# Kernel optimization log

Measured on AMD Instinct MI355X. Metric: run time of the kernel, lower is better.

Reference implementation:

```python
import jax, jax.numpy as jnp
import numpy as np

EPS = 1e-5


def gcn_conv(x, W, b, src, dst):
    """PyG GCNConv: transform, add self-loops, symmetric norm, scatter-add, bias."""
    N = x.shape[0]
    h = x @ W  # [N, out]
    loop = jnp.arange(N)
    s = jnp.concatenate([src, loop])  # sources incl. self-loops
    d = jnp.concatenate([dst, loop])  # targets incl. self-loops
    deg = jax.ops.segment_sum(jnp.ones(s.shape[0], h.dtype), d, num_segments=N)
    dis = jnp.where(deg > 0, jax.lax.rsqrt(deg), 0.0)  # deg^-1/2
    norm = dis[s] * dis[d]  # [E+N]
    out = jax.ops.segment_sum(h[s] * norm[:, None], d, num_segments=N)
    return out + b


def batchnorm(x, gamma, beta):
    mu = x.mean(axis=0)
    var = x.var(axis=0)
    return (x - mu) * jax.lax.rsqrt(var + EPS) * gamma + beta


def setup_inputs() -> dict:
    key = jax.random.key(0)
    ks = jax.random.split(key, 6)
    N, E = 100000, 1600000
    IN, HID, OUT = 128, 256, 64
    x = jax.random.normal(ks[0], (N, IN), dtype=jnp.float32)
    edge_index = jax.random.randint(ks[1], (2, E), 0, N, dtype=jnp.int64)
    W1 = jax.random.normal(ks[2], (IN, HID), dtype=jnp.float32) / np.sqrt(IN)
    b1 = jnp.zeros((HID,), jnp.float32)
    gamma1 = jnp.ones((HID,), jnp.float32)
    beta1 = jnp.zeros((HID,), jnp.float32)
    W2 = jax.random.normal(ks[3], (HID, OUT), dtype=jnp.float32) / np.sqrt(HID)
    b2 = jnp.zeros((OUT,), jnp.float32)
    return {"x": x, "edge_index": edge_index, "W1": W1, "b1": b1,
            "gamma1": gamma1, "beta1": beta1, "W2": W2, "b2": b2}


def reference(x, edge_index, W1, b1, gamma1, beta1, W2, b2):
    src, dst = edge_index[0], edge_index[1]
    h = gcn_conv(x, W1, b1, src, dst)
    h = jax.nn.relu(batchnorm(h, gamma1, beta1))
    # dropout is identity at inference
    return gcn_conv(h, W2, b2, src, dst)
```

## Files before the change

kernel.cpp:

```cpp
#include <hip/hip_runtime.h>
#include <hip/hip_bf16.h>


#define IN_F  128
#define HID_F 256
#define OUT_F 64
#define BK_SHIFT 8
#define BK_SIZE  256
#define CHUNK    8192
#define CAP      8192

typedef unsigned int uint;
typedef unsigned short ushort;
typedef short bf16x8 __attribute__((ext_vector_type(8)));
typedef float f32x4 __attribute__((ext_vector_type(4)));

__device__ __forceinline__ ushort f2bf(float f) {
    uint u = __float_as_uint(f);
    uint r = (u + 0x7fffu + ((u >> 16) & 1u)) >> 16;
    return (ushort)r;
}
__device__ __forceinline__ float bf_lo(uint u) { return __uint_as_float(u << 16); }
__device__ __forceinline__ float bf_hi(uint u) { return __uint_as_float(u & 0xffff0000u); }

#define ACC8(u)                                         \
    do {                                                \
        acc[0] += bf_lo((u).x); acc[1] += bf_hi((u).x); \
        acc[2] += bf_lo((u).y); acc[3] += bf_hi((u).y); \
        acc[4] += bf_lo((u).z); acc[5] += bf_hi((u).z); \
        acc[6] += bf_lo((u).w); acc[7] += bf_hi((u).w); \
    } while (0)


__global__ __launch_bounds__(512) void scatter_wprep_kernel(
        const int* __restrict__ src, const int* __restrict__ dst,
        int* __restrict__ bcursor, uint* __restrict__ ebuf,
        const float* __restrict__ W1, const float* __restrict__ W2,
        ushort* __restrict__ W1bp, ushort* __restrict__ W2bp,
        int E, int NB, int nchunk) {
    if (blockIdx.x >= nchunk) {
        int i = (blockIdx.x - nchunk) * 512 + threadIdx.x;
        if (i < 32768) {
            int kk = i & 31, c = (i >> 5) & 255, kc = i >> 13;
            W1bp[i] = f2bf(W1[(size_t)(kc * 32 + kk) * HID_F + c]);
        } else {
            int j = i - 32768;
            int kk = j & 31, c = (j >> 5) & 63, kc = j >> 11;
            W2bp[j] = f2bf(W2[(size_t)(kc * 32 + kk) * OUT_F + c]);
        }
        return;
    }
    __shared__ int h[512];
    __shared__ int cur[512];
    for (int i = threadIdx.x; i < NB; i += 512) h[i] = 0;
    __syncthreads();
    int base = blockIdx.x * CHUNK;
    int end = min(base + CHUNK, E);
    for (int i = base + threadIdx.x; i < end; i += 512)
        atomicAdd(&h[dst[i] >> BK_SHIFT], 1);
    __syncthreads();
    for (int i = threadIdx.x; i < NB; i += 512)
        cur[i] = i * CAP + (h[i] ? atomicAdd(&bcursor[i], h[i]) : 0);
    __syncthreads();
    for (int i = base + threadIdx.x; i < end; i += 512) {
        int d = dst[i], s = src[i];
        int b = d >> BK_SHIFT;
        int pos = atomicAdd(&cur[b], 1);
        ebuf[pos] = (uint)s | ((uint)(d & (BK_SIZE - 1)) << 24);
    }
}

__global__ __launch_bounds__(1024) void bucket_build_kernel(
        const uint* __restrict__ ebuf, const int* __restrict__ bcursor,
        int* __restrict__ deg_e, int* __restrict__ offsets,
        float* __restrict__ dis, int* __restrict__ ssrc, int N) {
    __shared__ int cnt[256], off[256], cur[256];
    int b = blockIdx.x;
    int t = threadIdx.x;
    if (t < 256) cnt[t] = 0;
    __syncthreads();
    int e0 = b * CAP;
    int e1 = e0 + min(bcursor[b], CAP);
    for (int i = e0 + t; i < e1; i += 1024)
        atomicAdd(&cnt[ebuf[i] >> 24], 1);
    __syncthreads();
    int v = (t < 256) ? cnt[t] : 0;
    int vpad = (v + 3) & ~3;
    if (t < 256) off[t] = vpad;
    __syncthreads();
    for (int o = 1; o < 256; o <<= 1) {
        int u = (t >= o && t < 256) ? off[t - o] : 0;
        __syncthreads();
        if (t < 256) off[t] += u;
        __syncthreads();
    }
    int base_pad = b * (CAP + 768);
    if (t < 256) {
        int excl = off[t] - vpad;
        int d = b * BK_SIZE + t;
        if (d < N) {
            deg_e[d] = vpad;
            offsets[d] = base_pad + excl;
            dis[d] = rsqrtf((float)(v + 1));
        }
        cur[t] = excl;
    }
    __syncthreads();
    for (int i = e0 + t; i < e1; i += 1024) {
        uint e = ebuf[i];
        int ld = e >> 24;
        int pos = atomicAdd(&cur[ld], 1);
        ssrc[base_pad + pos] = (int)(e & 0xFFFFFFu);
    }
    __syncthreads();
    if (t < 256) {
        int excl = off[t] - vpad;
        for (int i = v; i < vpad; i++)
            ssrc[base_pad + excl + i] = N;
    }
}

__global__ void xprep_kernel(const float* __restrict__ x, const float* __restrict__ dis,
                             uint* __restrict__ xs, int N) {
    int i = blockIdx.x * 256 + threadIdx.x;
    if (i < (N + 1) * 32) {
        int n = i >> 5;
        if (n >= N) { ((uint2*)xs)[i] = make_uint2(0u, 0u); return; }
        float dn = dis[n];
        float4 v = ((const float4*)x)[i];
        uint2 o;
        o.x = (uint)f2bf(dn * v.x) | ((uint)f2bf(dn * v.y) << 16);
        o.y = (uint)f2bf(dn * v.z) | ((uint)f2bf(dn * v.w) << 16);
        ((uint2*)xs)[i] = o;
    }
}


__global__ void aggx_kernel(const uint* __restrict__ xs, const int* __restrict__ ssrc,
                            const int* __restrict__ offsets, const int* __restrict__ deg_e,
                            const float* __restrict__ dis, uint* __restrict__ zb, int N) {
    int lane = threadIdx.x & 63;
    int n = blockIdx.x * 4 + (threadIdx.x >> 6);
    if (n >= N) return;
    int grp = lane >> 4;
    int ck = lane & 15;
    float acc[8];
#pragma unroll
    for (int i = 0; i < 8; i++) acc[i] = 0.f;
    int start = offsets[n], cnt = deg_e[n];
    for (int base = 0; base < cnt; base += 64) {
        int m = min(64, cnt - base);
        int idx = base + lane;
        int sv = ssrc[start + (idx < cnt ? idx : cnt - 1)];
        int rounds = m >> 2;
        int q = 0;
        for (; q + 4 <= rounds; q += 4) {
            int sA = __shfl(sv, ((q + 0) << 2) | grp);
            int sB = __shfl(sv, ((q + 1) << 2) | grp);
            int sC = __shfl(sv, ((q + 2) << 2) | grp);
            int sD = __shfl(sv, ((q + 3) << 2) | grp);
            uint4 uA = *(const uint4*)(xs + ((size_t)sA << 6) + (ck << 2));
            uint4 uB = *(const uint4*)(xs + ((size_t)sB << 6) + (ck << 2));
            uint4 uC = *(const uint4*)(xs + ((size_t)sC << 6) + (ck << 2));
            uint4 uD = *(const uint4*)(xs + ((size_t)sD << 6) + (ck << 2));
            ACC8(uA); ACC8(uB); ACC8(uC); ACC8(uD);
        }
        for (; q < rounds; q++) {
            int s = __shfl(sv, (q << 2) | grp);
            uint4 u = *(const uint4*)(xs + ((size_t)s << 6) + (ck << 2));
            ACC8(u);
        }
    }
#pragma unroll
    for (int i = 0; i < 8; i++) acc[i] += __shfl_down(acc[i], 32);
#pragma unroll
    for (int i = 0; i < 8; i++) acc[i] += __shfl_down(acc[i], 16);
    if (grp == 0) {
        uint4 u = *(const uint4*)(xs + ((size_t)n << 6) + (ck << 2));
        ACC8(u);
        float dn = dis[n];
        uint4 o;
        o.x = (uint)f2bf(dn * acc[0]) | ((uint)f2bf(dn * acc[1]) << 16);
        o.y = (uint)f2bf(dn * acc[2]) | ((uint)f2bf(dn * acc[3]) << 16);
        o.z = (uint)f2bf(dn * acc[4]) | ((uint)f2bf(dn * acc[5]) << 16);
        o.w = (uint)f2bf(dn * acc[6]) | ((uint)f2bf(dn * acc[7]) << 16);
        *(uint4*)(zb + ((size_t)n << 6) + (ck << 2)) = o;
    }
}

__global__ __launch_bounds__(256) void gemm1_kernel(const uint* __restrict__ zb,
                                                    const uint* __restrict__ W1bp,
                                                    const float* __restrict__ b1,
                                                    ushort* __restrict__ out1b,
                                                    float* __restrict__ bnp, int N) {
    __shared__ uint sbuf[8192];
    int t = threadIdx.x;
    int n0 = blockIdx.x * 64;
    for (int i = t; i < 64 * 16; i += 256) {
        int r = i >> 4, q = i & 15;
        int node = n0 + r;
        uint4 v = make_uint4(0u, 0u, 0u, 0u);
        if (node < N) v = *(const uint4*)(zb + (size_t)node * 64 + q * 4);
        int p = q ^ (r & 15);
        *(uint4*)(&sbuf[r * 64 + p * 4]) = v;
    }
    __syncthreads();
    int wave = t >> 6, lane = t & 63;
    int quad = lane >> 4, lrow = lane & 15;
    f32x4 acc[4][4];
#pragma unroll
    for (int m = 0; m < 4; m++)
#pragma unroll
        for (int nt = 0; nt < 4; nt++) acc[m][nt] = (f32x4)(0.f);
#pragma unroll
    for (int kc = 0; kc < 4; kc++) {
        bf16x8 bfr[4];
#pragma unroll
        for (int nt = 0; nt < 4; nt++) {
            int c = wave * 64 + nt * 16 + lrow;
            bfr[nt] = *(const bf16x8*)(W1bp + ((size_t)(kc * 256 + c) * 16 + quad * 4));
        }
        bf16x8 afr[4];
#pragma unroll
        for (int m = 0; m < 4; m++) {
            int p = (kc * 4 + quad) ^ lrow;
            afr[m] = *(const bf16x8*)(&sbuf[(m * 16 + lrow) * 64 + p * 4]);
        }
#pragma unroll
        for (int m = 0; m < 4; m++)
#pragma unroll
            for (int nt = 0; nt < 4; nt++)
                acc[m][nt] = __builtin_amdgcn_mfma_f32_16x16x32_bf16(
                    afr[m], bfr[nt], acc[m][nt], 0, 0, 0);
    }
    __syncthreads();
#pragma unroll
    for (int nt = 0; nt < 4; nt++) {
        int c = wave * 64 + nt * 16 + lrow;
        float bb = b1[c];
        float s = 0.f, q = 0.f;
#pragma unroll
        for (int m = 0; m < 4; m++) {
#pragma unroll
            for (int r = 0; r < 4; r++) {
                int row = m * 16 + quad * 4 + r;
                float v = acc[m][nt][r] + bb;
                if (n0 + row < N) { s += v; q = fmaf(v, v, q); }
                uint hv = (uint)f2bf(v);
                uint pv = __shfl_xor(hv, 1);
                if ((lrow & 1) == 0)
                    sbuf[row * 128 + (c >> 1)] = hv | (pv << 16);
            }
        }
        s += __shfl_down(s, 32); q += __shfl_down(q, 32);
        s += __shfl_down(s, 16); q += __shfl_down(q, 16);
        if (quad == 0) {
            bnp[(size_t)blockIdx.x * 512 + c] = s;
            bnp[(size_t)blockIdx.x * 512 + 256 + c] = q;
        }
    }
    __syncthreads();
    uint* out1g = (uint*)out1b;
    for (int i = t; i < 2048; i += 256) {
        int row = i >> 5;
        if (n0 + row < N)
            *(uint4*)(out1g + (size_t)(n0 + row) * 128 + (i & 31) * 4) =
                *(const uint4*)(&sbuf[i * 4]);
    }
}

__global__ void bnred_kernel(const float* __restrict__ bnp, float* __restrict__ bnsum,
                             int nblk) {
    int g = blockIdx.x, t = threadIdx.x;
    float s = 0.f, q = 0.f;
    for (int b = g; b < nblk; b += 32) {
        s += bnp[(size_t)b * 512 + t];
        q += bnp[(size_t)b * 512 + 256 + t];
    }
    atomicAdd(&bnsum[t], s);
    atomicAdd(&bnsum[256 + t], q);
}

__global__ __launch_bounds__(256) void gemm2_kernel(const ushort* __restrict__ out1b,
                                                    const uint* __restrict__ W2bp,
                                                    const float* __restrict__ dis,
                                                    const float* __restrict__ bnsum,
                                                    const float* __restrict__ gamma,
                                                    const float* __restrict__ beta,
                                                    ushort* __restrict__ gs, int N) {
    __shared__ uint sbuf[8192];
    __shared__ float bns[256], bnb[256];
    const uint* out1u = (const uint*)out1b;
    int t = threadIdx.x;
    int n0 = blockIdx.x * 64;
    if (blockIdx.x == 0 && t < 32) ((uint*)gs)[(size_t)N * 32 + t] = 0u;
    {
        float invN = 1.0f / (float)N;
        float mean = bnsum[t] * invN;
        float var = bnsum[256 + t] * invN - mean * mean;
        float sc = gamma[t] * rsqrtf(fmaxf(var, 0.f) + 1e-5f);
        bns[t] = sc;
        bnb[t] = beta[t] - mean * sc;
    }
    __syncthreads();
    for (int i = t; i < 64 * 32; i += 256) {
        int r = i >> 5, q = i & 31;
        int node = n0 + r;
        uint4 v = make_uint4(0u, 0u, 0u, 0u);
        if (node < N) {
            uint4 w = *(const uint4*)(out1u + (size_t)node * 128 + q * 4);
            int c0 = q * 8;
            float r0 = fmaxf(fmaf(bf_lo(w.x), bns[c0 + 0], bnb[c0 + 0]), 0.f);
            float r1 = fmaxf(fmaf(bf_hi(w.x), bns[c0 + 1], bnb[c0 + 1]), 0.f);
            float r2 = fmaxf(fmaf(bf_lo(w.y), bns[c0 + 2], bnb[c0 + 2]), 0.f);
            float r3 = fmaxf(fmaf(bf_hi(w.y), bns[c0 + 3], bnb[c0 + 3]), 0.f);
            float r4 = fmaxf(fmaf(bf_lo(w.z), bns[c0 + 4], bnb[c0 + 4]), 0.f);
            float r5 = fmaxf(fmaf(bf_hi(w.z), bns[c0 + 5], bnb[c0 + 5]), 0.f);
            float r6 = fmaxf(fmaf(bf_lo(w.w), bns[c0 + 6], bnb[c0 + 6]), 0.f);
            float r7 = fmaxf(fmaf(bf_hi(w.w), bns[c0 + 7], bnb[c0 + 7]), 0.f);
            v.x = (uint)f2bf(r0) | ((uint)f2bf(r1) << 16);
            v.y = (uint)f2bf(r2) | ((uint)f2bf(r3) << 16);
            v.z = (uint)f2bf(r4) | ((uint)f2bf(r5) << 16);
            v.w = (uint)f2bf(r6) | ((uint)f2bf(r7) << 16);
        }
        int p = (q & 16) | ((q & 15) ^ (r & 15));
        *(uint4*)(&sbuf[r * 128 + p * 4]) = v;
    }
    __syncthreads();
    int wave = t >> 6, lane = t & 63;
    int quad = lane >> 4, lrow = lane & 15;
    int c = wave * 16 + lrow;
    f32x4 acc[4];
#pragma unroll
    for (int m = 0; m < 4; m++) acc[m] = (f32x4)(0.f);
#pragma unroll
    for (int kc = 0; kc < 8; kc++) {
        bf16x8 bfr = *(const bf16x8*)(W2bp + ((size_t)(kc * 64 + c) * 16 + quad * 4));
#pragma unroll
        for (int m = 0; m < 4; m++) {
            int q = kc * 4 + quad;
            int p = (q & 16) | ((q & 15) ^ lrow);
            bf16x8 afr = *(const bf16x8*)(&sbuf[(m * 16 + lrow) * 128 + p * 4]);
            acc[m] = __builtin_amdgcn_mfma_f32_16x16x32_bf16(afr, bfr, acc[m], 0, 0, 0);
        }
    }
    __syncthreads();
#pragma unroll
    for (int m = 0; m < 4; m++) {
#pragma unroll
        for (int r = 0; r < 4; r++) {
            int row = m * 16 + quad * 4 + r;
            int node = n0 + row;
            float dn = (node < N) ? dis[node] : 0.f;
            uint hv = (uint)f2bf(dn * acc[m][r]);
            uint pv = __shfl_xor(hv, 1);
            if ((lrow & 1) == 0)
                sbuf[row * 32 + (c >> 1)] = hv | (pv << 16);
        }
    }
    __syncthreads();
    uint* gsg = (uint*)gs;
    for (int i = t; i < 512; i += 256) {
        int row = i >> 3;
        if (n0 + row < N)
            *(uint4*)(gsg + (size_t)(n0 + row) * 32 + (i & 7) * 4) =
                *(const uint4*)(&sbuf[i * 4]);
    }
}

__global__ void agg2_kernel(const uint* __restrict__ gs, const int* __restrict__ ssrc,
                            const int* __restrict__ offsets, const int* __restrict__ deg_e,
                            const float* __restrict__ dis, const float* __restrict__ b2,
                            float* __restrict__ out, int N) {
    int lane = threadIdx.x & 63;
    int half = lane >> 5;
    int hl = lane & 31;
    int grp = hl >> 3;
    int ck = hl & 7;
    int n = blockIdx.x * 8 + ((threadIdx.x >> 6) << 1) + half;
    if (n >= N) return;
    float acc[8];
#pragma unroll
    for (int i = 0; i < 8; i++) acc[i] = 0.f;
    int start = offsets[n], cnt = deg_e[n];
    int hbase = half << 5;
    for (int base = 0; base < cnt; base += 32) {
        int m = min(32, cnt - base);
        int idx = base + hl;
        int sv = ssrc[start + (idx < cnt ? idx : cnt - 1)];
        int rounds = m >> 2;
        int q = 0;
        for (; q + 2 <= rounds; q += 2) {
            int sA = __shfl(sv, hbase | ((q + 0) << 2) | grp);
            int sB = __shfl(sv, hbase | ((q + 1) << 2) | grp);
            uint4 uA = *(const uint4*)(gs + ((size_t)sA << 5) + (ck << 2));
            uint4 uB = *(const uint4*)(gs + ((size_t)sB << 5) + (ck << 2));
            ACC8(uA); ACC8(uB);
        }
        for (; q < rounds; q++) {
            int s = __shfl(sv, hbase | (q << 2) | grp);
            uint4 u = *(const uint4*)(gs + ((size_t)s << 5) + (ck << 2));
            ACC8(u);
        }
    }
#pragma unroll
    for (int i = 0; i < 8; i++) acc[i] += __shfl_down(acc[i], 16);
#pragma unroll
    for (int i = 0; i < 8; i++) acc[i] += __shfl_down(acc[i], 8);
    if (grp == 0) {
        uint4 u = *(const uint4*)(gs + ((size_t)n << 5) + (ck << 2));
        ACC8(u);
        float dn = dis[n];
        float4 bb0 = *(const float4*)(b2 + ck * 8);
        float4 bb1 = *(const float4*)(b2 + ck * 8 + 4);
        float* op = out + (size_t)n * OUT_F + ck * 8;
        *(float4*)op = make_float4(fmaf(dn, acc[0], bb0.x), fmaf(dn, acc[1], bb0.y),
                                   fmaf(dn, acc[2], bb0.z), fmaf(dn, acc[3], bb0.w));
        *(float4*)(op + 4) = make_float4(fmaf(dn, acc[4], bb1.x), fmaf(dn, acc[5], bb1.y),
                                         fmaf(dn, acc[6], bb1.z), fmaf(dn, acc[7], bb1.w));
    }
}

extern "C" void kernel_launch(void* const* d_in, const int* in_sizes, int n_in,
                              void* d_out, int out_size, void* d_ws, size_t ws_size,
                              hipStream_t stream) {
    const float* x      = (const float*)d_in[0];
    const int*   edges  = (const int*)d_in[1];
    const float* W1     = (const float*)d_in[2];
    const float* b1     = (const float*)d_in[3];
    const float* gamma1 = (const float*)d_in[4];
    const float* beta1  = (const float*)d_in[5];
    const float* W2     = (const float*)d_in[6];
    const float* b2     = (const float*)d_in[7];
    float* out = (float*)d_out;

    int N = in_sizes[0] / IN_F;
    int E = in_sizes[1] / 2;
    const int* src = edges;
    const int* dst = edges + E;
    int NB = (N + BK_SIZE - 1) / BK_SIZE;
    int nchunks = (E + CHUNK - 1) / CHUNK;
    int nblk1 = (N + 63) / 64;

    char* ws = (char*)d_ws;
    size_t off = 0;
    auto alloc = [&](size_t bytes) -> void* {
        void* p = ws + off;
        off += (bytes + 255) & ~(size_t)255;
        return p;
    };
    int*    deg_e   = (int*)alloc((size_t)N * 4);
    int*    offsets = (int*)alloc((size_t)N * 4);
    float*  dis     = (float*)alloc((size_t)(N + 1) * 4);
    int*    bcursor = (int*)alloc(512 * 4);
    float*  bnsum   = (float*)alloc(512 * 4);
    int*    ssrc    = (int*)alloc((size_t)NB * (CAP + 768) * 4);
    uint*   ebuf    = (uint*)alloc((size_t)NB * CAP * 4);
    uint*   xs      = (uint*)alloc((size_t)(N + 1) * (IN_F / 2) * 4);
    uint*   zb      = (uint*)alloc((size_t)N * (IN_F / 2) * 4);
    ushort* out1b   = (ushort*)alloc((size_t)N * HID_F * 2);
    float*  bnp     = (float*)alloc((size_t)nblk1 * 512 * 4);
    ushort* W1bp    = (ushort*)alloc(4 * 256 * 32 * 2);
    ushort* W2bp    = (ushort*)alloc(8 * 64 * 32 * 2);
    ushort* gs      = (ushort*)zb;

    hipMemsetAsync(bcursor, 0, 2 * 512 * 4, stream);

    scatter_wprep_kernel<<<nchunks + 96, 512, 0, stream>>>(src, dst, bcursor, ebuf,
                                                           W1, W2, W1bp, W2bp,
                                                           E, NB, nchunks);
    bucket_build_kernel<<<NB, 1024, 0, stream>>>(ebuf, bcursor, deg_e, offsets, dis, ssrc, N);
    xprep_kernel<<<((N + 1) * 32 + 255) / 256, 256, 0, stream>>>(x, dis, xs, N);
    aggx_kernel<<<(N + 3) / 4, 256, 0, stream>>>(xs, ssrc, offsets, deg_e, dis, zb, N);
    gemm1_kernel<<<nblk1, 256, 0, stream>>>(zb, (const uint*)W1bp, b1, out1b, bnp, N);
    bnred_kernel<<<32, 256, 0, stream>>>(bnp, bnsum, nblk1);
    gemm2_kernel<<<nblk1, 256, 0, stream>>>(out1b, (const uint*)W2bp, dis, bnsum,
                                            gamma1, beta1, gs, N);
    agg2_kernel<<<(N + 7) / 8, 256, 0, stream>>>((const uint*)gs, ssrc, offsets, deg_e, dis,
                                                 b2, out, N);
}
```

Before: 318.3 us.

## Split aggx feature dimension across two blocks with half-wave per node

Restructures the first-layer neighbor aggregation so each 32-lane half-wave handles one node and one half of the 128 bf16 features. Blocks are interleaved so the two feature halves of the same node octet land on adjacent block indices, and the self-row load is hoisted before the edge loop. This doubles node-level parallelism per wave and cuts per-node latency chains, at the cost of reading each node's edge index list twice and issuing narrower 64-byte gathers per row.

```diff
diff --git a/kernel.cpp b/kernel.cpp
--- a/kernel.cpp
+++ b/kernel.cpp
@@ -140,51 +140,57 @@
                             const int* __restrict__ offsets, const int* __restrict__ deg_e,
                             const float* __restrict__ dis, uint* __restrict__ zb, int N) {
     int lane = threadIdx.x & 63;
-    int n = blockIdx.x * 4 + (threadIdx.x >> 6);
+    int half = lane >> 5;
+    int hl = lane & 31;
+    int grp = hl >> 3;
+    int ck = hl & 7;
+    int j = blockIdx.x & 7;
+    int fo = (j >> 2) << 5;
+    int oct = ((blockIdx.x >> 3) << 2) + (j & 3);
+    int n = (oct << 3) + ((threadIdx.x >> 6) << 1) + half;
     if (n >= N) return;
-    int grp = lane >> 4;
-    int ck = lane & 15;
     float acc[8];
 #pragma unroll
     for (int i = 0; i < 8; i++) acc[i] = 0.f;
     int start = offsets[n], cnt = deg_e[n];
-    for (int base = 0; base < cnt; base += 64) {
-        int m = min(64, cnt - base);
-        int idx = base + lane;
+    uint4 uself = *(const uint4*)(xs + ((size_t)n << 6) + fo + (ck << 2));
+    int hbase = half << 5;
+    for (int base = 0; base < cnt; base += 32) {
+        int m = min(32, cnt - base);
+        int idx = base + hl;
         int sv = ssrc[start + (idx < cnt ? idx : cnt - 1)];
         int rounds = m >> 2;
         int q = 0;
         for (; q + 4 <= rounds; q += 4) {
-            int sA = __shfl(sv, ((q + 0) << 2) | grp);
-            int sB = __shfl(sv, ((q + 1) << 2) | grp);
-            int sC = __shfl(sv, ((q + 2) << 2) | grp);
-            int sD = __shfl(sv, ((q + 3) << 2) | grp);
-            uint4 uA = *(const uint4*)(xs + ((size_t)sA << 6) + (ck << 2));
-            uint4 uB = *(const uint4*)(xs + ((size_t)sB << 6) + (ck << 2));
-            uint4 uC = *(const uint4*)(xs + ((size_t)sC << 6) + (ck << 2));
-            uint4 uD = *(const uint4*)(xs + ((size_t)sD << 6) + (ck << 2));
+            int sA = __shfl(sv, hbase | ((q + 0) << 2) | grp);
+            int sB = __shfl(sv, hbase | ((q + 1) << 2) | grp);
+            int sC = __shfl(sv, hbase | ((q + 2) << 2) | grp);
+            int sD = __shfl(sv, hbase | ((q + 3) << 2) | grp);
+            uint4 uA = *(const uint4*)(xs + ((size_t)sA << 6) + fo + (ck << 2));
+            uint4 uB = *(const uint4*)(xs + ((size_t)sB << 6) + fo + (ck << 2));
+            uint4 uC = *(const uint4*)(xs + ((size_t)sC << 6) + fo + (ck << 2));
+            uint4 uD = *(const uint4*)(xs + ((size_t)sD << 6) + fo + (ck << 2));
             ACC8(uA); ACC8(uB); ACC8(uC); ACC8(uD);
         }
         for (; q < rounds; q++) {
-            int s = __shfl(sv, (q << 2) | grp);
-            uint4 u = *(const uint4*)(xs + ((size_t)s << 6) + (ck << 2));
+            int s = __shfl(sv, hbase | (q << 2) | grp);
+            uint4 u = *(const uint4*)(xs + ((size_t)s << 6) + fo + (ck << 2));
             ACC8(u);
         }
     }
 #pragma unroll
-    for (int i = 0; i < 8; i++) acc[i] += __shfl_down(acc[i], 32);
-#pragma unroll
     for (int i = 0; i < 8; i++) acc[i] += __shfl_down(acc[i], 16);
+#pragma unroll
+    for (int i = 0; i < 8; i++) acc[i] += __shfl_down(acc[i], 8);
     if (grp == 0) {
-        uint4 u = *(const uint4*)(xs + ((size_t)n << 6) + (ck << 2));
-        ACC8(u);
+        ACC8(uself);
         float dn = dis[n];
         uint4 o;
         o.x = (uint)f2bf(dn * acc[0]) | ((uint)f2bf(dn * acc[1]) << 16);
         o.y = (uint)f2bf(dn * acc[2]) | ((uint)f2bf(dn * acc[3]) << 16);
         o.z = (uint)f2bf(dn * acc[4]) | ((uint)f2bf(dn * acc[5]) << 16);
         o.w = (uint)f2bf(dn * acc[6]) | ((uint)f2bf(dn * acc[7]) << 16);
-        *(uint4*)(zb + ((size_t)n << 6) + (ck << 2)) = o;
+        *(uint4*)(zb + ((size_t)n << 6) + fo + (ck << 2)) = o;
     }
 }
 
@@ -471,7 +477,11 @@
                                                            E, NB, nchunks);
     bucket_build_kernel<<<NB, 1024, 0, stream>>>(ebuf, bcursor, deg_e, offsets, dis, ssrc, N);
     xprep_kernel<<<((N + 1) * 32 + 255) / 256, 256, 0, stream>>>(x, dis, xs, N);
-    aggx_kernel<<<(N + 3) / 4, 256, 0, stream>>>(xs, ssrc, offsets, deg_e, dis, zb, N);
+    {
+        int noct = (N + 7) >> 3;
+        int grid = ((noct + 3) >> 2) << 3;
+        aggx_kernel<<<grid, 256, 0, stream>>>(xs, ssrc, offsets, deg_e, dis, zb, N);
+    }
     gemm1_kernel<<<nblk1, 256, 0, stream>>>(zb, (const uint*)W1bp, b1, out1b, bnp, N);
     bnred_kernel<<<32, 256, 0, stream>>>(bnp, bnsum, nblk1);
     gemm2_kernel<<<nblk1, 256, 0, stream>>>(out1b, (const uint*)W2bp, dis, bnsum,
```

New measurement: 313.1 us. Within noise of the previous version (-1.6%).
